# Kernel tuning notes

Hardware: AMD Instinct MI355X
Metric: run time of the kernel (lower is better)

## Reference

```python
import jax, jax.numpy as jnp
import numpy as np

B, S, D, DK, DV, H, DH, L, V = 2, 1024, 1024, 64, 64, 16, 4096, 8, 256


def setup_inputs() -> dict:
    key = jax.random.key(0)
    ks = jax.random.split(key, 20)
    sd = 0.02
    inp = {
        "tokens": jax.random.randint(ks[0], (B, S), 0, V, dtype=jnp.int32),
        "emb": sd * jax.random.normal(ks[1], (V, D), jnp.float32),
        "pos": sd * jax.random.normal(ks[2], (S, D), jnp.float32),
        # per-layer stacked params; Linear stored as [in, out] (x @ W + b)
        "Wq": sd * jax.random.normal(ks[3], (L, D, H * DK), jnp.float32),
        "bq": jnp.zeros((L, H * DK), jnp.float32),
        "Wk": sd * jax.random.normal(ks[4], (L, D, H * DK), jnp.float32),
        "bk": jnp.zeros((L, H * DK), jnp.float32),
        "Wv": sd * jax.random.normal(ks[5], (L, D, H * DV), jnp.float32),
        "bv": jnp.zeros((L, H * DV), jnp.float32),
        "Wo": sd * jax.random.normal(ks[6], (L, H * DV, D), jnp.float32),  # no bias
        "W1": sd * jax.random.normal(ks[7], (L, D, DH), jnp.float32),
        "b1": jnp.zeros((L, DH), jnp.float32),
        "W2": sd * jax.random.normal(ks[8], (L, DH, D), jnp.float32),
        "b2": jnp.zeros((L, D), jnp.float32),
        "Wr": sd * jax.random.normal(ks[9], (D, V), jnp.float32),
        "br": jnp.zeros((V,), jnp.float32),
    }
    return inp


def _forward(tokens, emb, pos, Wq, bq, Wk, bk, Wv, bv, Wo, W1, b1, W2, b2, Wr, br):
    x = emb[tokens] + pos  # [B,S,D]
    # additive causal mask exactly as Mask('causal'): 1 - 1/tril -> 0 below diag, -inf above
    tril = jnp.tril(jnp.ones((S, S), jnp.float32))
    addmask = 1.0 - 1.0 / tril  # [S,S]
    scale = 1.0 / np.sqrt(DK)

    def layer(x, p):
        wq, bq_, wk, bk_, wv, bv_, wo, w1, b1_, w2, b2_ = p
        q = (x @ wq + bq_).reshape(B, S, H, DK).transpose(0, 2, 1, 3)
        k = (x @ wk + bk_).reshape(B, S, H, DK).transpose(0, 2, 1, 3)
        v = (x @ wv + bv_).reshape(B, S, H, DV).transpose(0, 2, 1, 3)
        scores = jnp.einsum('bhqd,bhkd->bhqk', q * scale, k) + addmask
        a = jax.nn.softmax(scores, axis=-1)
        o = jnp.einsum('bhqk,bhkd->bhqd', a, v)  # [B,H,S,DV]
        o = o.transpose(0, 2, 1, 3).reshape(B, S, H * DV)
        h = x + o @ wo  # residual after attention
        mlp = jax.nn.gelu(h @ w1 + b1_, approximate=False) @ w2 + b2_
        return h + mlp, None

    params = (Wq, bq, Wk, bk, Wv, bv, Wo, W1, b1, W2, b2)
    x, _ = jax.lax.scan(layer, x, params)
    return x @ Wr + br  # [B,S,V]


def reference(tokens, emb, pos, Wq, bq, Wk, bk, Wv, bv, Wo, W1, b1, W2, b2, Wr, br):
    return _forward(tokens, emb, pos, Wq, bq, Wk, bk, Wv, bv, Wo, W1, b1, W2, b2, Wr, br)
```

## Files before the change

kernel.cpp:

```cpp
#include <hip/hip_runtime.h>
#include <cstdint>
#include <cstddef>

#define B_ 2
#define S_ 1024
#define D_ 1024
#define H_ 16
#define DK_ 64
#define DH_ 4096
#define L_ 8
#define V_ 256
#define M_ROWS 2048

typedef unsigned short u16;
typedef __bf16 bf16x8 __attribute__((ext_vector_type(8)));
typedef float f32x4 __attribute__((ext_vector_type(4)));

__device__ __forceinline__ u16 f2b(float f) {
  union { float f; uint32_t u; } v; v.f = f;
  uint32_t u = v.u;
  return (u16)((u + 0x7FFFu + ((u >> 16) & 1u)) >> 16);
}
__device__ __forceinline__ float b2f(u16 h) {
  union { uint32_t u; float f; } v; v.u = ((uint32_t)h) << 16;
  return v.f;
}

__device__ __forceinline__ void load16_lds(const void* g, void* l) {
  __builtin_amdgcn_global_load_lds(
      (const __attribute__((address_space(1))) unsigned int*)g,
      (__attribute__((address_space(3))) unsigned int*)l, 16, 0, 0);
}

__global__ void embed_kernel(const int* __restrict__ tokens, const float* __restrict__ emb,
                             const float* __restrict__ pos, float* __restrict__ xf,
                             u16* __restrict__ xb) {
  int row = blockIdx.x;
  int s = row & (S_ - 1);
  int tok = tokens[row];
  const float* e = emb + (size_t)tok * D_;
  const float* p = pos + (size_t)s * D_;
#pragma unroll
  for (int i = 0; i < D_ / 256; i++) {
    int d = threadIdx.x + i * 256;
    float v = e[d] + p[d];
    xf[(size_t)row * D_ + d] = v;
    xb[(size_t)row * D_ + d] = f2b(v);
  }
}

__global__ void convT_kernel(const float* __restrict__ W, u16* __restrict__ Wt, int K, int N) {
  __shared__ float tile[32][33];
  int n0 = blockIdx.x * 32, k0 = blockIdx.y * 32;
  int tx = threadIdx.x & 31, ty = threadIdx.x >> 5;
#pragma unroll
  for (int i = 0; i < 4; i++)
    tile[ty + i * 8][tx] = W[(size_t)(k0 + ty + i * 8) * N + n0 + tx];
  __syncthreads();
#pragma unroll
  for (int i = 0; i < 4; i++)
    Wt[(size_t)(n0 + ty + i * 8) * K + k0 + tx] = f2b(tile[tx][ty + i * 8]);
}

__global__ void convAll_kernel(const float* __restrict__ Wq, const float* __restrict__ Wk,
                               const float* __restrict__ Wv, const float* __restrict__ Wo,
                               const float* __restrict__ W1, const float* __restrict__ W2,
                               int l, u16* __restrict__ WqT, u16* __restrict__ WoT,
                               u16* __restrict__ W1T, u16* __restrict__ W2T) {
  int t = blockIdx.x;
  const float* src; u16* dst; int K, N, bx, by;
  if (t < 3072) {
    int which = t >> 10, t2 = t & 1023;
    src = (which == 0 ? Wq : which == 1 ? Wk : Wv) + (size_t)l * (1u << 20);
    dst = WqT + (size_t)which * (1u << 20);
    K = 1024; N = 1024; bx = t2 & 31; by = t2 >> 5;
  } else if (t < 4096) {
    int t2 = t - 3072;
    src = Wo + (size_t)l * (1u << 20); dst = WoT;
    K = 1024; N = 1024; bx = t2 & 31; by = t2 >> 5;
  } else if (t < 8192) {
    int t2 = t - 4096;
    src = W1 + (size_t)l * (4u << 20); dst = W1T;
    K = 1024; N = 4096; bx = t2 & 127; by = t2 >> 7;
  } else {
    int t2 = t - 8192;
    src = W2 + (size_t)l * (4u << 20); dst = W2T;
    K = 4096; N = 1024; bx = t2 & 31; by = t2 >> 5;
  }
  __shared__ float tile[32][33];
  int n0 = bx * 32, k0 = by * 32;
  int tx = threadIdx.x & 31, ty = threadIdx.x >> 5;
#pragma unroll
  for (int i = 0; i < 4; i++)
    tile[ty + i * 8][tx] = src[(size_t)(k0 + ty + i * 8) * N + n0 + tx];
  __syncthreads();
#pragma unroll
  for (int i = 0; i < 4; i++)
    dst[(size_t)(n0 + ty + i * 8) * K + k0 + tx] = f2b(tile[tx][ty + i * 8]);
}

__global__ __launch_bounds__(256, 2) void flash_kernel(
    const u16* __restrict__ qb, const u16* __restrict__ kb,
    const u16* __restrict__ vT, u16* __restrict__ ob) {
  int qt = (int)(gridDim.x - 1) - (int)blockIdx.x;
  int bh = blockIdx.y;
  int b = bh >> 4, h = bh & 15;
  int tid = threadIdx.x, lane = tid & 63, w = tid >> 6;
  int l16 = lane & 15, quad = lane >> 4;

  __shared__ u16 sQ[64][72];
  __shared__ u16 sK[128][72];
  __shared__ u16 sV[64][136];
  __shared__ u16 sP[4][16][136];

  {
    int row = tid >> 2;
    int c0 = (tid & 3) * 16;
    const u16* g = qb + ((size_t)(b * S_ + qt * 64 + row)) * 1024 + h * 64 + c0;
#pragma unroll
    for (int c = 0; c < 2; c++) {
      union { uint4 v; u16 h[8]; } u;
      u.v = *(const uint4*)(g + c * 8);
#pragma unroll
      for (int j = 0; j < 8; j++) u.h[j] = f2b(b2f(u.h[j]) * 0.125f);
      *(uint4*)&sQ[row][c0 + c * 8] = u.v;
    }
  }

  f32x4 accO[4];
#pragma unroll
  for (int i = 0; i < 4; i++) { f32x4 z = {0.f, 0.f, 0.f, 0.f}; accO[i] = z; }
  float mrow[4], lrow[4];
#pragma unroll
  for (int r = 0; r < 4; r++) { mrow[r] = -1e30f; lrow[r] = 0.f; }

  int ktmax = qt >> 1;
  for (int kt = 0; kt <= ktmax; kt++) {
    {
      int row = tid >> 1, c0 = (tid & 1) * 32;
      const u16* g = kb + ((size_t)(b * S_ + kt * 128 + row)) * 1024 + h * 64;
#pragma unroll
      for (int c = 0; c < 4; c++)
        *(uint4*)&sK[row][c0 + c * 8] = *(const uint4*)(g + c0 + c * 8);
      int rv = tid >> 2, cv0 = (tid & 3) * 32;
      const u16* gv = vT + ((size_t)(bh * 64 + rv)) * 1024 + kt * 128;
#pragma unroll
      for (int c = 0; c < 4; c++)
        *(uint4*)&sV[rv][cv0 + c * 8] = *(const uint4*)(gv + cv0 + c * 8);
    }
    __syncthreads();

    f32x4 accS[8];
#pragma unroll
    for (int ni = 0; ni < 8; ni++) { f32x4 z = {0.f, 0.f, 0.f, 0.f}; accS[ni] = z; }
#pragma unroll
    for (int kk = 0; kk < 2; kk++) {
      bf16x8 a = *(const bf16x8*)&sQ[w * 16 + l16][kk * 32 + quad * 8];
#pragma unroll
      for (int ni = 0; ni < 8; ni++) {
        bf16x8 bb = *(const bf16x8*)&sK[ni * 16 + l16][kk * 32 + quad * 8];
        accS[ni] = __builtin_amdgcn_mfma_f32_16x16x32_bf16(a, bb, accS[ni], 0, 0, 0);
      }
    }
    int qw0 = qt * 64 + w * 16;
    if (kt * 128 + 127 > qw0) {
#pragma unroll
      for (int ni = 0; ni < 8; ni++) {
        int kv = kt * 128 + ni * 16 + l16;
#pragma unroll
        for (int r = 0; r < 4; r++)
          if (kv > qw0 + quad * 4 + r) accS[ni][r] = -1e30f;
      }
    }
    float alpha[4];
#pragma unroll
    for (int r = 0; r < 4; r++) {
      float m = accS[0][r];
#pragma unroll
      for (int ni = 1; ni < 8; ni++) m = fmaxf(m, accS[ni][r]);
#pragma unroll
      for (int off = 1; off < 16; off <<= 1) m = fmaxf(m, __shfl_xor(m, off, 64));
      float mn = fmaxf(mrow[r], m);
      alpha[r] = __expf(mrow[r] - mn);
      mrow[r] = mn;
    }
    float sum[4] = {0.f, 0.f, 0.f, 0.f};
#pragma unroll
    for (int ni = 0; ni < 8; ni++) {
#pragma unroll
      for (int r = 0; r < 4; r++) {
        float p = __expf(accS[ni][r] - mrow[r]);
        sum[r] += p;
        sP[w][quad * 4 + r][ni * 16 + l16] = f2b(p);
      }
    }
#pragma unroll
    for (int r = 0; r < 4; r++) {
#pragma unroll
      for (int off = 1; off < 16; off <<= 1) sum[r] += __shfl_xor(sum[r], off, 64);
      lrow[r] = lrow[r] * alpha[r] + sum[r];
#pragma unroll
      for (int ni = 0; ni < 4; ni++) accO[ni][r] *= alpha[r];
    }
    __syncthreads();
#pragma unroll
    for (int kk2 = 0; kk2 < 4; kk2++) {
      bf16x8 a = *(const bf16x8*)&sP[w][l16][kk2 * 32 + quad * 8];
#pragma unroll
      for (int ni = 0; ni < 4; ni++) {
        bf16x8 bb = *(const bf16x8*)&sV[ni * 16 + l16][kk2 * 32 + quad * 8];
        accO[ni] = __builtin_amdgcn_mfma_f32_16x16x32_bf16(a, bb, accO[ni], 0, 0, 0);
      }
    }
    __syncthreads();
  }
  u16* orow = ob + ((size_t)(b * S_ + qt * 64 + w * 16 + quad * 4)) * 1024 + h * 64;
#pragma unroll
  for (int r = 0; r < 4; r++) {
    float inv = 1.0f / lrow[r];
#pragma unroll
    for (int ni = 0; ni < 4; ni++)
      orow[(size_t)r * 1024 + ni * 16 + l16] = f2b(accO[ni][r] * inv);
  }
}

enum { M_PLAIN = 0, M_QKV = 1 };

template <int MODE, bool BIAS, bool GELU, bool RESID, bool WF32, bool WBF16>
__global__ __launch_bounds__(256, 2) void gemm_kernel(
    const u16* __restrict__ A, const u16* __restrict__ Bbase,
    const float* __restrict__ bias0, const float* __restrict__ bias1,
    const float* __restrict__ bias2, const float* __restrict__ resid,
    float* __restrict__ Cf, u16* __restrict__ Cb, u16* __restrict__ vTout,
    int M, int N, int K, int ldA, int ldB, int ldC) {
  int bn = blockIdx.x, bm = blockIdx.y, z = blockIdx.z;
  const u16* Bt = Bbase;
  const float* bias = bias0;
  u16* cb = Cb;
  if (MODE == M_QKV) {
    Bt = Bbase + (size_t)z * (1u << 20);
    bias = (z == 0) ? bias0 : (z == 1) ? bias1 : bias2;
    cb = Cb + (size_t)z * ((size_t)M_ROWS * 1024);
  }
  int tid = threadIdx.x;
  int lane = tid & 63, w = tid >> 6;
  int l16 = lane & 15, quad = lane >> 4;
  int wm = w >> 1, wn = w & 1;
  int m0 = bm * 128, n0 = bn * 128;
  int rsub = lane >> 3, csw = lane & 7;

  __shared__ u16 smem[16384];

  f32x4 acc[4][4];
#pragma unroll
  for (int i = 0; i < 4; i++)
#pragma unroll
    for (int j = 0; j < 4; j++) { f32x4 zv = {0.f, 0.f, 0.f, 0.f}; acc[i][j] = zv; }

  int rowA = w * 32 + rsub;
  int swsrc = (csw ^ (rowA & 7)) << 3;
  const u16* gA = A + (size_t)(m0 + rowA) * ldA + swsrc;
  const u16* gB = Bt + (size_t)(n0 + rowA) * ldB + swsrc;
  int swz = l16 & 7;

  for (int k0 = 0; k0 < K; k0 += 64) {
#pragma unroll
    for (int i = 0; i < 4; i++) {
      load16_lds(gA + (size_t)(i * 8) * ldA + k0, &smem[(w * 32 + i * 8) * 64]);
      load16_lds(gB + (size_t)(i * 8) * ldB + k0, &smem[8192 + (w * 32 + i * 8) * 64]);
    }
    __syncthreads();
#pragma unroll
    for (int kk = 0; kk < 2; kk++) {
      bf16x8 af[4], bfr[4];
#pragma unroll
      for (int mi = 0; mi < 4; mi++)
        af[mi] = *(const bf16x8*)&smem[(wm * 64 + mi * 16 + l16) * 64 +
                                       (((kk * 4 + quad) ^ swz) << 3)];
#pragma unroll
      for (int ni = 0; ni < 4; ni++)
        bfr[ni] = *(const bf16x8*)&smem[8192 + (wn * 64 + ni * 16 + l16) * 64 +
                                        (((kk * 4 + quad) ^ swz) << 3)];
#pragma unroll
      for (int mi = 0; mi < 4; mi++)
#pragma unroll
        for (int ni = 0; ni < 4; ni++)
          acc[mi][ni] = __builtin_amdgcn_mfma_f32_16x16x32_bf16(af[mi], bfr[ni],
                                                                acc[mi][ni], 0, 0, 0);
    }
    __syncthreads();
  }

  if (MODE == M_QKV && z == 2) {
#pragma unroll
    for (int mi = 0; mi < 4; mi++) {
      int sl = wm * 64 + mi * 16 + quad * 4;
#pragma unroll
      for (int ni = 0; ni < 4; ni++) {
        int dl = wn * 64 + ni * 16 + l16;
        float bv = bias[n0 + dl];
        union { u16 h[4]; uint2 u; } pk;
#pragma unroll
        for (int r = 0; r < 4; r++) pk.h[r] = f2b(acc[mi][ni][r] + bv);
        int phys = ((((sl >> 3) ^ (dl & 7)) << 3) | (sl & 7));
        *(uint2*)&smem[dl * 128 + phys] = pk.u;
      }
    }
    __syncthreads();
    {
      int drow = tid >> 1;
      int b = m0 >> 10;
      int gcol = n0 + drow;
      u16* dst = vTout + ((size_t)((b * 16 + (gcol >> 6)) * 64 + (gcol & 63))) * 1024 +
                 (m0 & 1023);
#pragma unroll
      for (int i = 0; i < 8; i++) {
        int sc = (tid & 1) * 8 + i;
        int phys = sc ^ (drow & 7);
        *(uint4*)(dst + sc * 8) = *(const uint4*)&smem[drow * 128 + phys * 8];
      }
    }
    return;
  }

#pragma unroll
  for (int mi = 0; mi < 4; mi++)
#pragma unroll
    for (int ni = 0; ni < 4; ni++) {
      int col = n0 + wn * 64 + ni * 16 + l16;
      float bv = BIAS ? bias[col] : 0.f;
#pragma unroll
      for (int r = 0; r < 4; r++) {
        int row = m0 + wm * 64 + mi * 16 + quad * 4 + r;
        float v = acc[mi][ni][r] + bv;
        if (RESID) v += resid[(size_t)row * ldC + col];
        if (GELU) v = 0.5f * v * (1.f + erff(v * 0.70710678118f));
        if (WF32) Cf[(size_t)row * ldC + col] = v;
        if (WBF16) cb[(size_t)row * ldC + col] = f2b(v);
      }
    }
}

extern "C" void kernel_launch(void* const* d_in, const int* in_sizes, int n_in,
                              void* d_out, int out_size, void* d_ws, size_t ws_size,
                              hipStream_t stream) {
  const int*   tokens = (const int*)d_in[0];
  const float* emb = (const float*)d_in[1];
  const float* pos = (const float*)d_in[2];
  const float* Wq  = (const float*)d_in[3];
  const float* bq  = (const float*)d_in[4];
  const float* Wk  = (const float*)d_in[5];
  const float* bk  = (const float*)d_in[6];
  const float* Wv  = (const float*)d_in[7];
  const float* bv  = (const float*)d_in[8];
  const float* Wo  = (const float*)d_in[9];
  const float* W1  = (const float*)d_in[10];
  const float* b1  = (const float*)d_in[11];
  const float* W2  = (const float*)d_in[12];
  const float* b2  = (const float*)d_in[13];
  const float* Wr  = (const float*)d_in[14];
  const float* br  = (const float*)d_in[15];
  float* out = (float*)d_out;

  char* ws = (char*)d_ws;
  size_t off = 0;
  auto alloc = [&](size_t bytes) {
    char* p = ws + off;
    off += (bytes + 255) & ~(size_t)255;
    return p;
  };
  float* xf  = (float*)alloc((size_t)M_ROWS * 1024 * 4);
  float* hf  = (float*)alloc((size_t)M_ROWS * 1024 * 4);
  u16*  xb   = (u16*)alloc((size_t)M_ROWS * 1024 * 2);
  u16*  hb   = (u16*)alloc((size_t)M_ROWS * 1024 * 2);
  u16*  qkb  = (u16*)alloc((size_t)2 * M_ROWS * 1024 * 2);
  u16*  vT   = (u16*)alloc((size_t)M_ROWS * 1024 * 2);
  u16*  ob   = (u16*)alloc((size_t)M_ROWS * 1024 * 2);
  u16*  tmid = (u16*)alloc((size_t)M_ROWS * DH_ * 2);
  u16*  Wt   = (u16*)alloc((size_t)12 * 1024 * 1024 * 2);
  u16*  WrT  = (u16*)alloc((size_t)V_ * 1024 * 2);
  (void)ws_size; (void)in_sizes; (void)n_in; (void)out_size;

  u16* WqT = Wt;
  u16* WoT = Wt + (size_t)3 * 1024 * 1024;
  u16* W1T = Wt + (size_t)4 * 1024 * 1024;
  u16* W2T = Wt + (size_t)8 * 1024 * 1024;

  embed_kernel<<<dim3(M_ROWS), 256, 0, stream>>>(tokens, emb, pos, xf, xb);

  for (int l = 0; l < L_; l++) {
    convAll_kernel<<<dim3(12288), 256, 0, stream>>>(Wq, Wk, Wv, Wo, W1, W2, l,
                                                    WqT, WoT, W1T, W2T);
    gemm_kernel<M_QKV, true, false, false, false, true><<<dim3(8, 16, 3), 256, 0, stream>>>(
        xb, WqT, bq + l * 1024, bk + l * 1024, bv + l * 1024, nullptr,
        nullptr, qkb, vT, M_ROWS, 1024, 1024, 1024, 1024, 1024);
    flash_kernel<<<dim3(16, 32), 256, 0, stream>>>(qkb, qkb + (size_t)M_ROWS * 1024, vT, ob);
    gemm_kernel<M_PLAIN, false, false, true, true, true><<<dim3(8, 16), 256, 0, stream>>>(
        ob, WoT, nullptr, nullptr, nullptr, xf,
        hf, hb, nullptr, M_ROWS, 1024, 1024, 1024, 1024, 1024);
    gemm_kernel<M_PLAIN, true, true, false, false, true><<<dim3(32, 16), 256, 0, stream>>>(
        hb, W1T, b1 + l * DH_, nullptr, nullptr, nullptr,
        nullptr, tmid, nullptr, M_ROWS, DH_, 1024, 1024, 1024, DH_);
    gemm_kernel<M_PLAIN, true, false, true, true, true><<<dim3(8, 16), 256, 0, stream>>>(
        tmid, W2T, b2 + l * 1024, nullptr, nullptr, hf,
        xf, xb, nullptr, M_ROWS, 1024, DH_, DH_, DH_, 1024);
  }

  convT_kernel<<<dim3(8, 32), 256, 0, stream>>>(Wr, WrT, 1024, V_);
  gemm_kernel<M_PLAIN, true, false, false, true, false><<<dim3(2, 16), 256, 0, stream>>>(
      xb, WrT, br, nullptr, nullptr, nullptr,
      out, nullptr, nullptr, M_ROWS, V_, 1024, 1024, 1024, V_);
}
```

Before: 1.765 ms.

## Hoist weight conversion, split-K the W2 GEMM, and use smaller tiles for narrow GEMMs

```diff
diff --git a/kernel.cpp b/kernel.cpp
--- a/kernel.cpp
+++ b/kernel.cpp
@@ -49,43 +49,38 @@
   }
 }
 
-__global__ void convT_kernel(const float* __restrict__ W, u16* __restrict__ Wt, int K, int N) {
-  __shared__ float tile[32][33];
-  int n0 = blockIdx.x * 32, k0 = blockIdx.y * 32;
-  int tx = threadIdx.x & 31, ty = threadIdx.x >> 5;
-#pragma unroll
-  for (int i = 0; i < 4; i++)
-    tile[ty + i * 8][tx] = W[(size_t)(k0 + ty + i * 8) * N + n0 + tx];
-  __syncthreads();
-#pragma unroll
-  for (int i = 0; i < 4; i++)
-    Wt[(size_t)(n0 + ty + i * 8) * K + k0 + tx] = f2b(tile[tx][ty + i * 8]);
-}
-
-__global__ void convAll_kernel(const float* __restrict__ Wq, const float* __restrict__ Wk,
-                               const float* __restrict__ Wv, const float* __restrict__ Wo,
-                               const float* __restrict__ W1, const float* __restrict__ W2,
-                               int l, u16* __restrict__ WqT, u16* __restrict__ WoT,
-                               u16* __restrict__ W1T, u16* __restrict__ W2T) {
+__global__ void convAllLayers_kernel(const float* __restrict__ Wq, const float* __restrict__ Wk,
+                                     const float* __restrict__ Wv, const float* __restrict__ Wo,
+                                     const float* __restrict__ W1, const float* __restrict__ W2,
+                                     const float* __restrict__ Wr,
+                                     u16* __restrict__ Wt, u16* __restrict__ WrT) {
   int t = blockIdx.x;
   const float* src; u16* dst; int K, N, bx, by;
-  if (t < 3072) {
-    int which = t >> 10, t2 = t & 1023;
-    src = (which == 0 ? Wq : which == 1 ? Wk : Wv) + (size_t)l * (1u << 20);
-    dst = WqT + (size_t)which * (1u << 20);
-    K = 1024; N = 1024; bx = t2 & 31; by = t2 >> 5;
-  } else if (t < 4096) {
-    int t2 = t - 3072;
-    src = Wo + (size_t)l * (1u << 20); dst = WoT;
-    K = 1024; N = 1024; bx = t2 & 31; by = t2 >> 5;
-  } else if (t < 8192) {
-    int t2 = t - 4096;
-    src = W1 + (size_t)l * (4u << 20); dst = W1T;
-    K = 1024; N = 4096; bx = t2 & 127; by = t2 >> 7;
+  if (t < 98304) {
+    int l = t / 12288, s = t % 12288;
+    u16* slab = Wt + (size_t)l * (12u << 20);
+    if (s < 3072) {
+      int which = s >> 10, t2 = s & 1023;
+      src = (which == 0 ? Wq : which == 1 ? Wk : Wv) + (size_t)l * (1u << 20);
+      dst = slab + (size_t)which * (1u << 20);
+      K = 1024; N = 1024; bx = t2 & 31; by = t2 >> 5;
+    } else if (s < 4096) {
+      int t2 = s - 3072;
+      src = Wo + (size_t)l * (1u << 20); dst = slab + (3u << 20);
+      K = 1024; N = 1024; bx = t2 & 31; by = t2 >> 5;
+    } else if (s < 8192) {
+      int t2 = s - 4096;
+      src = W1 + (size_t)l * (4u << 20); dst = slab + (4u << 20);
+      K = 1024; N = 4096; bx = t2 & 127; by = t2 >> 7;
+    } else {
+      int t2 = s - 8192;
+      src = W2 + (size_t)l * (4u << 20); dst = slab + (8u << 20);
+      K = 4096; N = 1024; bx = t2 & 31; by = t2 >> 5;
+    }
   } else {
-    int t2 = t - 8192;
-    src = W2 + (size_t)l * (4u << 20); dst = W2T;
-    K = 4096; N = 1024; bx = t2 & 31; by = t2 >> 5;
+    int t2 = t - 98304;
+    src = Wr; dst = WrT;
+    K = 1024; N = 256; bx = t2 & 7; by = t2 >> 3;
   }
   __shared__ float tile[32][33];
   int n0 = bx * 32, k0 = by * 32;
@@ -226,13 +221,22 @@
 
 enum { M_PLAIN = 0, M_QKV = 1 };
 
-template <int MODE, bool BIAS, bool GELU, bool RESID, bool WF32, bool WBF16>
+template <int BM_, int BN_, int MODE, bool BIAS, bool GELU, bool RESID, bool WF32,
+          bool WBF16, int KSPLIT>
 __global__ __launch_bounds__(256, 2) void gemm_kernel(
     const u16* __restrict__ A, const u16* __restrict__ Bbase,
     const float* __restrict__ bias0, const float* __restrict__ bias1,
     const float* __restrict__ bias2, const float* __restrict__ resid,
     float* __restrict__ Cf, u16* __restrict__ Cb, u16* __restrict__ vTout,
     int M, int N, int K, int ldA, int ldB, int ldC) {
+  constexpr int WAVES_M = (BM_ == 128) ? 2 : 1;
+  constexpr int WAVES_N = 4 / WAVES_M;
+  constexpr int WM = BM_ / WAVES_M;
+  constexpr int WN = BN_ / WAVES_N;
+  constexpr int MI = WM / 16;
+  constexpr int NI = WN / 16;
+  constexpr int ASZ = BM_ * 64;
+
   int bn = blockIdx.x, bm = blockIdx.y, z = blockIdx.z;
   const u16* Bt = Bbase;
   const float* bias = bias0;
@@ -242,49 +246,54 @@
     bias = (z == 0) ? bias0 : (z == 1) ? bias1 : bias2;
     cb = Cb + (size_t)z * ((size_t)M_ROWS * 1024);
   }
+  int kz = (KSPLIT > 1) ? z : 0;
+  int k0beg = kz * (K / KSPLIT), k0end = k0beg + K / KSPLIT;
+
   int tid = threadIdx.x;
   int lane = tid & 63, w = tid >> 6;
   int l16 = lane & 15, quad = lane >> 4;
-  int wm = w >> 1, wn = w & 1;
-  int m0 = bm * 128, n0 = bn * 128;
+  int wm = (WAVES_M == 2) ? (w >> 1) : 0;
+  int wn = (WAVES_M == 2) ? (w & 1) : w;
+  int m0 = bm * BM_, n0 = bn * BN_;
   int rsub = lane >> 3, csw = lane & 7;
 
-  __shared__ u16 smem[16384];
-
-  f32x4 acc[4][4];
-#pragma unroll
-  for (int i = 0; i < 4; i++)
-#pragma unroll
-    for (int j = 0; j < 4; j++) { f32x4 zv = {0.f, 0.f, 0.f, 0.f}; acc[i][j] = zv; }
-
-  int rowA = w * 32 + rsub;
-  int swsrc = (csw ^ (rowA & 7)) << 3;
-  const u16* gA = A + (size_t)(m0 + rowA) * ldA + swsrc;
-  const u16* gB = Bt + (size_t)(n0 + rowA) * ldB + swsrc;
+  __shared__ u16 smem[(BM_ + BN_) * 64];
+
+  f32x4 acc[MI][NI];
+#pragma unroll
+  for (int i = 0; i < MI; i++)
+#pragma unroll
+    for (int j = 0; j < NI; j++) { f32x4 zv = {0.f, 0.f, 0.f, 0.f}; acc[i][j] = zv; }
+
+  int rowA = w * (BM_ / 4) + rsub;
+  int rowB = w * (BN_ / 4) + rsub;
+  const u16* gA = A + (size_t)(m0 + rowA) * ldA + ((csw ^ (rowA & 7)) << 3);
+  const u16* gB = Bt + (size_t)(n0 + rowB) * ldB + ((csw ^ (rowB & 7)) << 3);
   int swz = l16 & 7;
 
-  for (int k0 = 0; k0 < K; k0 += 64) {
-#pragma unroll
-    for (int i = 0; i < 4; i++) {
-      load16_lds(gA + (size_t)(i * 8) * ldA + k0, &smem[(w * 32 + i * 8) * 64]);
-      load16_lds(gB + (size_t)(i * 8) * ldB + k0, &smem[8192 + (w * 32 + i * 8) * 64]);
-    }
+  for (int k0 = k0beg; k0 < k0end; k0 += 64) {
+#pragma unroll
+    for (int i = 0; i < BM_ / 32; i++)
+      load16_lds(gA + (size_t)(i * 8) * ldA + k0, &smem[(w * (BM_ / 4) + i * 8) * 64]);
+#pragma unroll
+    for (int i = 0; i < BN_ / 32; i++)
+      load16_lds(gB + (size_t)(i * 8) * ldB + k0, &smem[ASZ + (w * (BN_ / 4) + i * 8) * 64]);
     __syncthreads();
 #pragma unroll
     for (int kk = 0; kk < 2; kk++) {
-      bf16x8 af[4], bfr[4];
-#pragma unroll
-      for (int mi = 0; mi < 4; mi++)
-        af[mi] = *(const bf16x8*)&smem[(wm * 64 + mi * 16 + l16) * 64 +
+      bf16x8 af[MI], bfr[NI];
+#pragma unroll
+      for (int mi = 0; mi < MI; mi++)
+        af[mi] = *(const bf16x8*)&smem[(wm * WM + mi * 16 + l16) * 64 +
                                        (((kk * 4 + quad) ^ swz) << 3)];
 #pragma unroll
-      for (int ni = 0; ni < 4; ni++)
-        bfr[ni] = *(const bf16x8*)&smem[8192 + (wn * 64 + ni * 16 + l16) * 64 +
+      for (int ni = 0; ni < NI; ni++)
+        bfr[ni] = *(const bf16x8*)&smem[ASZ + (wn * WN + ni * 16 + l16) * 64 +
                                         (((kk * 4 + quad) ^ swz) << 3)];
 #pragma unroll
-      for (int mi = 0; mi < 4; mi++)
-#pragma unroll
-        for (int ni = 0; ni < 4; ni++)
+      for (int mi = 0; mi < MI; mi++)
+#pragma unroll
+        for (int ni = 0; ni < NI; ni++)
           acc[mi][ni] = __builtin_amdgcn_mfma_f32_16x16x32_bf16(af[mi], bfr[ni],
                                                                 acc[mi][ni], 0, 0, 0);
     }
@@ -293,11 +302,11 @@
 
   if (MODE == M_QKV && z == 2) {
 #pragma unroll
-    for (int mi = 0; mi < 4; mi++) {
-      int sl = wm * 64 + mi * 16 + quad * 4;
-#pragma unroll
-      for (int ni = 0; ni < 4; ni++) {
-        int dl = wn * 64 + ni * 16 + l16;
+    for (int mi = 0; mi < MI; mi++) {
+      int sl = wm * WM + mi * 16 + quad * 4;
+#pragma unroll
+      for (int ni = 0; ni < NI; ni++) {
+        int dl = wn * WN + ni * 16 + l16;
         float bv = bias[n0 + dl];
         union { u16 h[4]; uint2 u; } pk;
 #pragma unroll
@@ -323,22 +332,43 @@
     return;
   }
 
-#pragma unroll
-  for (int mi = 0; mi < 4; mi++)
-#pragma unroll
-    for (int ni = 0; ni < 4; ni++) {
-      int col = n0 + wn * 64 + ni * 16 + l16;
+  float* cf = Cf;
+  if (KSPLIT > 1) cf = Cf + (size_t)kz * ((size_t)M * ldC);
+#pragma unroll
+  for (int mi = 0; mi < MI; mi++)
+#pragma unroll
+    for (int ni = 0; ni < NI; ni++) {
+      int col = n0 + wn * WN + ni * 16 + l16;
       float bv = BIAS ? bias[col] : 0.f;
 #pragma unroll
       for (int r = 0; r < 4; r++) {
-        int row = m0 + wm * 64 + mi * 16 + quad * 4 + r;
+        int row = m0 + wm * WM + mi * 16 + quad * 4 + r;
         float v = acc[mi][ni][r] + bv;
         if (RESID) v += resid[(size_t)row * ldC + col];
         if (GELU) v = 0.5f * v * (1.f + erff(v * 0.70710678118f));
-        if (WF32) Cf[(size_t)row * ldC + col] = v;
+        if (WF32) cf[(size_t)row * ldC + col] = v;
         if (WBF16) cb[(size_t)row * ldC + col] = f2b(v);
       }
     }
+}
+
+__global__ void reduce4_kernel(const float* __restrict__ part, const float* __restrict__ hf,
+                               const float* __restrict__ b2, float* __restrict__ xf,
+                               u16* __restrict__ xb) {
+  int idx = (blockIdx.x * 256 + threadIdx.x) * 4;
+  const size_t NT = (size_t)M_ROWS * 1024;
+  float4 a = *(const float4*)(hf + idx);
+  float4 bb = *(const float4*)(b2 + (idx & 1023));
+  a.x += bb.x; a.y += bb.y; a.z += bb.z; a.w += bb.w;
+#pragma unroll
+  for (int z = 0; z < 4; z++) {
+    float4 p = *(const float4*)(part + (size_t)z * NT + idx);
+    a.x += p.x; a.y += p.y; a.z += p.z; a.w += p.w;
+  }
+  *(float4*)(xf + idx) = a;
+  union { u16 h[4]; uint2 u; } pk;
+  pk.h[0] = f2b(a.x); pk.h[1] = f2b(a.y); pk.h[2] = f2b(a.z); pk.h[3] = f2b(a.w);
+  *(uint2*)(xb + idx) = pk.u;
 }
 
 extern "C" void kernel_launch(void* const* d_in, const int* in_sizes, int n_in,
@@ -369,45 +399,51 @@
     off += (bytes + 255) & ~(size_t)255;
     return p;
   };
-  float* xf  = (float*)alloc((size_t)M_ROWS * 1024 * 4);
-  float* hf  = (float*)alloc((size_t)M_ROWS * 1024 * 4);
-  u16*  xb   = (u16*)alloc((size_t)M_ROWS * 1024 * 2);
-  u16*  hb   = (u16*)alloc((size_t)M_ROWS * 1024 * 2);
-  u16*  qkb  = (u16*)alloc((size_t)2 * M_ROWS * 1024 * 2);
-  u16*  vT   = (u16*)alloc((size_t)M_ROWS * 1024 * 2);
-  u16*  ob   = (u16*)alloc((size_t)M_ROWS * 1024 * 2);
-  u16*  tmid = (u16*)alloc((size_t)M_ROWS * DH_ * 2);
-  u16*  Wt   = (u16*)alloc((size_t)12 * 1024 * 1024 * 2);
-  u16*  WrT  = (u16*)alloc((size_t)V_ * 1024 * 2);
+  float* xf   = (float*)alloc((size_t)M_ROWS * 1024 * 4);
+  float* hf   = (float*)alloc((size_t)M_ROWS * 1024 * 4);
+  float* part = (float*)alloc((size_t)4 * M_ROWS * 1024 * 4);
+  u16*  xb    = (u16*)alloc((size_t)M_ROWS * 1024 * 2);
+  u16*  hb    = (u16*)alloc((size_t)M_ROWS * 1024 * 2);
+  u16*  qkb   = (u16*)alloc((size_t)2 * M_ROWS * 1024 * 2);
+  u16*  vT    = (u16*)alloc((size_t)M_ROWS * 1024 * 2);
+  u16*  ob    = (u16*)alloc((size_t)M_ROWS * 1024 * 2);
+  u16*  tmid  = (u16*)alloc((size_t)M_ROWS * DH_ * 2);
+  u16*  Wt    = (u16*)alloc((size_t)8 * 12 * 1024 * 1024 * 2);
+  u16*  WrT   = (u16*)alloc((size_t)V_ * 1024 * 2);
   (void)ws_size; (void)in_sizes; (void)n_in; (void)out_size;
 
-  u16* WqT = Wt;
-  u16* WoT = Wt + (size_t)3 * 1024 * 1024;
-  u16* W1T = Wt + (size_t)4 * 1024 * 1024;
-  u16* W2T = Wt + (size_t)8 * 1024 * 1024;
-
   embed_kernel<<<dim3(M_ROWS), 256, 0, stream>>>(tokens, emb, pos, xf, xb);
+  convAllLayers_kernel<<<dim3(98560), 256, 0, stream>>>(Wq, Wk, Wv, Wo, W1, W2, Wr, Wt, WrT);
 
   for (int l = 0; l < L_; l++) {
-    convAll_kernel<<<dim3(12288), 256, 0, stream>>>(Wq, Wk, Wv, Wo, W1, W2, l,
-                                                    WqT, WoT, W1T, W2T);
-    gemm_kernel<M_QKV, true, false, false, false, true><<<dim3(8, 16, 3), 256, 0, stream>>>(
+    u16* slab = Wt + (size_t)l * (12u << 20);
+    u16* WqT = slab;
+    u16* WoT = slab + (3u << 20);
+    u16* W1T = slab + (4u << 20);
+    u16* W2T = slab + (8u << 20);
+
+    gemm_kernel<128, 128, M_QKV, true, false, false, false, true, 1>
+        <<<dim3(8, 16, 3), 256, 0, stream>>>(
         xb, WqT, bq + l * 1024, bk + l * 1024, bv + l * 1024, nullptr,
         nullptr, qkb, vT, M_ROWS, 1024, 1024, 1024, 1024, 1024);
     flash_kernel<<<dim3(16, 32), 256, 0, stream>>>(qkb, qkb + (size_t)M_ROWS * 1024, vT, ob);
-    gemm_kernel<M_PLAIN, false, false, true, true, true><<<dim3(8, 16), 256, 0, stream>>>(
+    gemm_kernel<64, 128, M_PLAIN, false, false, true, true, true, 1>
+        <<<dim3(8, 32), 256, 0, stream>>>(
         ob, WoT, nullptr, nullptr, nullptr, xf,
         hf, hb, nullptr, M_ROWS, 1024, 1024, 1024, 1024, 1024);
-    gemm_kernel<M_PLAIN, true, true, false, false, true><<<dim3(32, 16), 256, 0, stream>>>(
+    gemm_kernel<128, 128, M_PLAIN, true, true, false, false, true, 1>
+        <<<dim3(32, 16), 256, 0, stream>>>(
         hb, W1T, b1 + l * DH_, nullptr, nullptr, nullptr,
         nullptr, tmid, nullptr, M_ROWS, DH_, 1024, 1024, 1024, DH_);
-    gemm_kernel<M_PLAIN, true, false, true, true, true><<<dim3(8, 16), 256, 0, stream>>>(
-        tmid, W2T, b2 + l * 1024, nullptr, nullptr, hf,
-        xf, xb, nullptr, M_ROWS, 1024, DH_, DH_, DH_, 1024);
-  }
-
-  convT_kernel<<<dim3(8, 32), 256, 0, stream>>>(Wr, WrT, 1024, V_);
-  gemm_kernel<M_PLAIN, true, false, false, true, false><<<dim3(2, 16), 256, 0, stream>>>(
+    gemm_kernel<128, 128, M_PLAIN, false, false, false, true, false, 4>
+        <<<dim3(8, 16, 4), 256, 0, stream>>>(
+        tmid, W2T, nullptr, nullptr, nullptr, nullptr,
+        part, nullptr, nullptr, M_ROWS, 1024, DH_, DH_, DH_, 1024);
+    reduce4_kernel<<<dim3(2048), 256, 0, stream>>>(part, hf, b2 + l * 1024, xf, xb);
+  }
+
+  gemm_kernel<64, 128, M_PLAIN, true, false, false, true, false, 1>
+      <<<dim3(2, 32), 256, 0, stream>>>(
       xb, WrT, br, nullptr, nullptr, nullptr,
       out, nullptr, nullptr, M_ROWS, V_, 1024, 1024, 1024, V_);
 }
```

Result: faster. 1.686 ms (-4.5%).
